# Kernel optimization log

Hardware: AMD Instinct MI355X
Metric: run time of the kernel (lower is better)

## Reference

```python
import jax, jax.numpy as jnp
import numpy as np

EMBED_DIM = 1024
FFN_DIM = 4096
N_QUBITS = 16
BATCH, SEQ = 4, 2048


def setup_inputs() -> dict:
    key = jax.random.key(0)
    ks = jax.random.split(key, 6)
    s1 = 1.0 / np.sqrt(EMBED_DIM)
    s2 = 1.0 / np.sqrt(FFN_DIM)
    s3 = 1.0 / np.sqrt(N_QUBITS)
    return {
        "x": jax.random.normal(ks[0], (BATCH, SEQ, EMBED_DIM), jnp.float32),
        "W1": jax.random.normal(ks[1], (FFN_DIM, EMBED_DIM), jnp.float32) * s1,
        "Wq": jax.random.normal(ks[2], (N_QUBITS, FFN_DIM), jnp.float32) * s2,
        "theta": jax.random.normal(ks[3], (N_QUBITS,), jnp.float32),
        "W2": jax.random.normal(ks[4], (FFN_DIM, N_QUBITS), jnp.float32) * s3,
        "Wo": jax.random.normal(ks[5], (EMBED_DIM, FFN_DIM), jnp.float32) * s2,
    }


def reference(x, W1, Wq, theta, W2, Wo):
    # linear1: [b,s,e] @ [f,e]^T -> [b,s,f]
    h = jnp.einsum('bse,fe->bsf', x, W1)
    # to_qubits: [b,s,f] -> [b,s,q]
    q = jnp.einsum('bsf,qf->bsq', h, Wq)
    # Quantum circuit: RX(q_i) encoding then trainable RX(theta_i) per wire,
    # wires are unentangled product states -> <Z_i> = cos(q_i + theta_i).
    qm = jnp.cos(q + theta)
    # linear2 + relu
    h2 = jax.nn.relu(jnp.einsum('bsq,fq->bsf', qm, W2))
    # out_proj (dropout is identity in eval / p=0)
    return jnp.einsum('bsf,ef->bse', h2, Wo)
```

## Files before the change

kernel.cpp:

```cpp
#include <hip/hip_runtime.h>
#include <hip/hip_bf16.h>
#include <math.h>

typedef _Float16 f16;
typedef __attribute__((ext_vector_type(8))) _Float16 f16x8;
typedef __attribute__((ext_vector_type(4))) _Float16 f16x4;
typedef __attribute__((ext_vector_type(4))) float f32x4;

#define M_TOT 8192
#define E_DIM 1024
#define F_DIM 4096
#define NQ    16

#define BARRIER() asm volatile("s_barrier" ::: "memory")
#define WAITV(n)  asm volatile("s_waitcnt vmcnt(" #n ")" ::: "memory")
#define WAITLGKM() asm volatile("s_waitcnt lgkmcnt(0)" ::: "memory")

__device__ __forceinline__ f16x8 cvt8(float4 a, float4 b) {
    f16x8 o;
    o[0] = (f16)a.x; o[1] = (f16)a.y; o[2] = (f16)a.z; o[3] = (f16)a.w;
    o[4] = (f16)b.x; o[5] = (f16)b.y; o[6] = (f16)b.z; o[7] = (f16)b.w;
    return o;
}

__global__ __launch_bounds__(256) void prep_kernel(
    const float* __restrict__ W1, f16* __restrict__ W1t,
    const float* __restrict__ wo, f16* __restrict__ woh,
    const float* __restrict__ W2, f16* __restrict__ w2p)
{
    __shared__ float ls[64][68];
    const int b = blockIdx.x;
    if (b < 1024) {
        const int bf = b & 63;
        const int be = b >> 6;
        const int t  = threadIdx.x;
        const int r  = t >> 4;
        const int c4 = (t & 15) * 4;
        #pragma unroll
        for (int i = 0; i < 4; ++i) {
            int fr = r + i * 16;
            float4 v = *reinterpret_cast<const float4*>(W1 + (size_t)(bf * 64 + fr) * E_DIM + be * 64 + c4);
            ls[fr][c4] = v.x; ls[fr][c4 + 1] = v.y; ls[fr][c4 + 2] = v.z; ls[fr][c4 + 3] = v.w;
        }
        __syncthreads();
        const int er = t >> 2;
        const int fc = (t & 3) * 16;
        f16x8 o0, o1;
        #pragma unroll
        for (int j = 0; j < 8; ++j) { o0[j] = (f16)ls[fc + j][er]; o1[j] = (f16)ls[fc + 8 + j][er]; }
        f16* dst = W1t + (size_t)(be * 64 + er) * F_DIM + bf * 64 + fc;
        *reinterpret_cast<f16x8*>(dst)     = o0;
        *reinterpret_cast<f16x8*>(dst + 8) = o1;
    } else if (b < 3072) {
        size_t i = ((size_t)(b - 1024) * 256 + threadIdx.x) * 8;
        float4 v0 = *reinterpret_cast<const float4*>(wo + i);
        float4 v1 = *reinterpret_cast<const float4*>(wo + i + 4);
        *reinterpret_cast<f16x8*>(woh + i) = cvt8(v0, v1);
    } else {
        int t = (b - 3072) * 256 + threadIdx.x;
        size_t i = (size_t)t * 8;
        int col = (int)(i & 31);
        f16x8 o;
        if (col < NQ) {
            int row = (int)(i >> 5);
            float4 v0 = *reinterpret_cast<const float4*>(W2 + (size_t)row * NQ + col);
            float4 v1 = *reinterpret_cast<const float4*>(W2 + (size_t)row * NQ + col + 4);
            o = cvt8(v0, v1);
        } else {
            for (int k = 0; k < 8; ++k) o[k] = (f16)0.f;
        }
        *reinterpret_cast<f16x8*>(w2p + i) = o;
    }
}

__global__ __launch_bounds__(256) void tg_kernel(
    const float* __restrict__ Wq, const f16* __restrict__ W1t,
    float* __restrict__ pT)
{
    const int w = threadIdx.x >> 6, lane = threadIdx.x & 63;
    const int fr = lane & 15, fq = lane >> 4;
    const int kc = blockIdx.x & 15;
    const int et = blockIdx.x >> 4;
    const int e0 = et * 128 + w * 32;
    const int kbase = kc * 256;

    f32x4 acc[2] = {};
    #pragma unroll
    for (int s = 0; s < 8; ++s) {
        int k = kbase + s * 32 + fq * 8;
        float4 a0 = *reinterpret_cast<const float4*>(Wq + (size_t)fr * F_DIM + k);
        float4 a1 = *reinterpret_cast<const float4*>(Wq + (size_t)fr * F_DIM + k + 4);
        f16x8 af = cvt8(a0, a1);
        #pragma unroll
        for (int n = 0; n < 2; ++n) {
            f16x8 bf = *reinterpret_cast<const f16x8*>(W1t + (size_t)(e0 + n * 16 + fr) * F_DIM + k);
            acc[n] = __builtin_amdgcn_mfma_f32_16x16x32_f16(af, bf, acc[n], 0, 0, 0);
        }
    }
    #pragma unroll
    for (int n = 0; n < 2; ++n)
        #pragma unroll
        for (int j = 0; j < 4; ++j)
            pT[(size_t)kc * (16 * E_DIM) + (size_t)(fq * 4 + j) * E_DIM + e0 + n * 16 + fr] = acc[n][j];
}

__global__ __launch_bounds__(256) void treduce_kernel(
    const float* __restrict__ pT, f16* __restrict__ Th)
{
    int idx = blockIdx.x * 256 + threadIdx.x;
    float s = 0.f;
    #pragma unroll
    for (int kc = 0; kc < 16; ++kc) s += pT[(size_t)kc * (16 * E_DIM) + idx];
    Th[idx] = (f16)s;
}

__global__ __launch_bounds__(512) void qx2_kernel(
    const float* __restrict__ x, const f16* __restrict__ Th,
    const float* __restrict__ theta, f16* __restrict__ qmp)
{
    __shared__ __align__(16) f16 ths[16 * 1024];
    __shared__ float pql[2048];
    const int tid = threadIdx.x, w = tid >> 6, lane = tid & 63;
    const int fr = lane & 15, fq = lane >> 4;
    const int m0 = blockIdx.x * 64;

    #pragma unroll
    for (int i = 0; i < 4; ++i) {
        int tau = i * 512 + tid;
        int q   = tau >> 7;
        int kb  = tau & 127;
        f16x8 v = *reinterpret_cast<const f16x8*>(Th + (size_t)q * E_DIM + kb * 8);
        int boff = (q * 2048 + kb * 16) ^ ((q & 7) << 4);
        *reinterpret_cast<f16x8*>((char*)ths + boff) = v;
    }
    __syncthreads();

    const int kc = w >> 2;
    const int rg = w & 3;
    const float* xa = x + (size_t)(m0 + rg * 16 + fr) * E_DIM + kc * 512;
    f32x4 acc = {};
    #pragma unroll
    for (int s = 0; s < 16; ++s) {
        int ko = s * 32 + fq * 8;
        float4 a0 = *reinterpret_cast<const float4*>(xa + ko);
        float4 a1 = *reinterpret_cast<const float4*>(xa + ko + 4);
        f16x8 af = cvt8(a0, a1);
        int boff = (fr * 2048 + (kc * 512 + ko) * 2) ^ ((fr & 7) << 4);
        f16x8 bf = *reinterpret_cast<const f16x8*>((char*)ths + boff);
        acc = __builtin_amdgcn_mfma_f32_16x16x32_f16(af, bf, acc, 0, 0, 0);
    }
    #pragma unroll
    for (int j = 0; j < 4; ++j)
        pql[(kc * 64 + rg * 16 + fq * 4 + j) * 16 + fr] = acc[j];
    __syncthreads();

    #pragma unroll
    for (int e = 0; e < 2; ++e) {
        int idx = e * 512 + tid;
        int row = idx >> 4, q = idx & 15;
        float s = pql[idx] + pql[1024 + idx];
        float v = cosf(s + theta[q]);
        qmp[(size_t)(m0 + row) * 32 + q]      = (f16)v;
        qmp[(size_t)(m0 + row) * 32 + 16 + q] = (f16)0.f;
    }
}

__device__ __forceinline__ void gload_lds16(const f16* g, f16* l) {
    __builtin_amdgcn_global_load_lds(
        (const __attribute__((address_space(1))) void*)(g),
        (__attribute__((address_space(3))) void*)(l), 16, 0, 0);
}

__global__ __launch_bounds__(512, 2)
void gemm4f(const f16* __restrict__ qmp, const f16* __restrict__ w2p,
            const f16* __restrict__ Wo, f16* __restrict__ P0, f16* __restrict__ P1)
{
    extern __shared__ __align__(16) f16 smem[];
    const int tid  = threadIdx.x;
    const int w    = tid >> 6;
    const int lane = tid & 63;

    const int bid = blockIdx.x;
    const int bx    = bid & 3;
    const int split = (bid >> 2) & 1;
    const int by    = bid >> 3;
    const int m0 = by * 256, n0 = bx * 256;

    const int wr = w >> 2, wc = w & 3;
    const int fr = lane & 15, fq = lane >> 4;
    const int K = 2048;

    const f16* Bb  = Wo + (size_t)split * K;
    const f16* w2g = w2p + (size_t)split * K * 32;
    f16* Pout = split ? P1 : P0;

    const int r0w = w * 32 + fr;
    f16x8 qreg0 = *reinterpret_cast<const f16x8*>(qmp + (size_t)(m0 + r0w) * 32 + fq * 8);
    f16x8 qreg1 = *reinterpret_cast<const f16x8*>(qmp + (size_t)(m0 + r0w + 16) * 32 + fq * 8);

    const int rl   = w * 8 + (lane >> 3);
    const int scol = (((lane & 7) ^ (rl & 7)) * 8);
    const f16* gB = Bb + (size_t)(n0 + rl) * F_DIM + scol;
    f16* lB = smem + 16384 + w * 512;

#define SB(b,h,j,kt) gload_lds16(gB + (size_t)((h)*128 + (j)*64) * F_DIM + (kt), lB + (b)*32768 + (h)*8192 + (j)*4096)
#define SBH(b,h,kt) do { SB(b,h,0,kt); SB(b,h,1,kt); } while(0)

    f16x8 w2a[4], w2b[4];
#define LOADW2(R, kt) do { _Pragma("unroll") \
    for (int ft = 0; ft < 4; ++ft) \
        R[ft] = *reinterpret_cast<const f16x8*>(w2g + (size_t)((kt) + ft*16 + fr) * 32 + fq * 8); } while(0)

#define PRODUCE(bdst, W2R) do {                                                   \
    f32x4 z_ = {0.f, 0.f, 0.f, 0.f};                                              \
    _Pragma("unroll") for (int ft = 0; ft < 4; ++ft) {                            \
        f32x4 c0_ = __builtin_amdgcn_mfma_f32_16x16x32_f16(W2R[ft], qreg0, z_, 0, 0, 0); \
        f32x4 c1_ = __builtin_amdgcn_mfma_f32_16x16x32_f16(W2R[ft], qreg1, z_, 0, 0, 0); \
        f16x4 h0_, h1_;                                                           \
        _Pragma("unroll") for (int jj = 0; jj < 4; ++jj) {                        \
            h0_[jj] = (f16)fmaxf(c0_[jj], 0.f); h1_[jj] = (f16)fmaxf(c1_[jj], 0.f); } \
        const int sl_ = (2 * ft + (fq >> 1)) ^ (fr & 7);                          \
        *reinterpret_cast<f16x4*>(smem + (bdst)*32768 + (r0w)*64      + sl_*8 + ((fq & 1) << 2)) = h0_; \
        *reinterpret_cast<f16x4*>(smem + (bdst)*32768 + (r0w+16)*64   + sl_*8 + ((fq & 1) << 2)) = h1_; \
    } } while(0)

    const int xm  = fr & 7;
    const int so0 = ((0 + fq) ^ xm) * 8;
    const int so1 = ((4 + fq) ^ xm) * 8;
    const int aro = (wr * 128 + fr) * 64;
    const int bro = (wc * 64  + fr) * 64;

#define AF(b,m,ks) (*reinterpret_cast<const f16x8*>(smem + (b)*32768 + aro + (m)*1024 + so##ks))
#define BF(b,n,ks) (*reinterpret_cast<const f16x8*>(smem + (b)*32768 + 16384 + bro + (n)*1024 + so##ks))

    f32x4 acc[8][4] = {};
    f16x8 bf[4][2];

#define PHASE(b, p, STAGES, W4) do {                                              \
    f16x8 a00 = AF(b, 2*(p),   0), a01 = AF(b, 2*(p),   1);                       \
    f16x8 a10 = AF(b, 2*(p)+1, 0), a11 = AF(b, 2*(p)+1, 1);                       \
    if ((p) == 0) { _Pragma("unroll")                                             \
        for (int n = 0; n < 4; ++n) { bf[n][0] = BF(b,n,0); bf[n][1] = BF(b,n,1); } } \
    STAGES;                                                                       \
    BARRIER();                                                                    \
    __builtin_amdgcn_s_setprio(1);                                                \
    _Pragma("unroll") for (int n = 0; n < 4; ++n) {                               \
        acc[2*(p)  ][n] = __builtin_amdgcn_mfma_f32_16x16x32_f16(a00, bf[n][0], acc[2*(p)  ][n], 0,0,0); \
        acc[2*(p)+1][n] = __builtin_amdgcn_mfma_f32_16x16x32_f16(a10, bf[n][0], acc[2*(p)+1][n], 0,0,0); } \
    _Pragma("unroll") for (int n = 0; n < 4; ++n) {                               \
        acc[2*(p)  ][n] = __builtin_amdgcn_mfma_f32_16x16x32_f16(a01, bf[n][1], acc[2*(p)  ][n], 0,0,0); \
        acc[2*(p)+1][n] = __builtin_amdgcn_mfma_f32_16x16x32_f16(a11, bf[n][1], acc[2*(p)+1][n], 0,0,0); } \
    __builtin_amdgcn_s_setprio(0);                                                \
    if (W4) { WAITV(8); WAITLGKM(); }                                             \
    BARRIER(); } while(0)

    const int NT = K >> 6;
    const int NI = NT >> 1;

    LOADW2(w2b, 0);
    LOADW2(w2a, 64);
    SBH(0,0,0);  SBH(0,1,0);
    SBH(1,0,64); SBH(1,1,64);
    WAITV(0);
    BARRIER();
    PRODUCE(0, w2b);
    WAITLGKM();
    BARRIER();

    for (int i = 0; i < NI; ++i) {
        int t2 = 2*i+2; if (t2 > NT-1) t2 = NT-1;
        int t3 = 2*i+3; if (t3 > NT-1) t3 = NT-1;
        const int k2 = t2 << 6, k3 = t3 << 6;
        PHASE(0, 0, PRODUCE(1, w2a),            0);
        PHASE(0, 1, LOADW2(w2b, k2); SBH(0,0,k2), 0);
        PHASE(0, 2, SBH(0,1,k2),                0);
        PHASE(0, 3, ,                           1);
        PHASE(1, 0, PRODUCE(0, w2b),            0);
        PHASE(1, 1, LOADW2(w2a, k3); SBH(1,0,k3), 0);
        PHASE(1, 2, SBH(1,1,k3),                0);
        PHASE(1, 3, ,                           1);
    }
    WAITV(0);

    #pragma unroll
    for (int m = 0; m < 8; ++m) {
        #pragma unroll
        for (int n = 0; n < 4; ++n) {
            #pragma unroll
            for (int j = 0; j < 4; ++j) {
                int row = m0 + wr * 128 + m * 16 + fq * 4 + j;
                int col = n0 + wc * 64  + n * 16 + fr;
                Pout[(size_t)row * E_DIM + col] = (f16)acc[m][n][j];
            }
        }
    }
#undef SB
#undef SBH
#undef LOADW2
#undef PRODUCE
#undef AF
#undef BF
#undef PHASE
}

__global__ __launch_bounds__(256) void out_reduce2_kernel(
    float* __restrict__ out, const f16* __restrict__ p0, const f16* __restrict__ p1)
{
    size_t i = ((size_t)blockIdx.x * 256 + threadIdx.x) * 8;
    f16x8 a = *reinterpret_cast<const f16x8*>(p0 + i);
    f16x8 b = *reinterpret_cast<const f16x8*>(p1 + i);
    float4 v0, v1;
    v0.x = (float)a[0] + (float)b[0]; v0.y = (float)a[1] + (float)b[1];
    v0.z = (float)a[2] + (float)b[2]; v0.w = (float)a[3] + (float)b[3];
    v1.x = (float)a[4] + (float)b[4]; v1.y = (float)a[5] + (float)b[5];
    v1.z = (float)a[6] + (float)b[6]; v1.w = (float)a[7] + (float)b[7];
    *reinterpret_cast<float4*>(out + i)     = v0;
    *reinterpret_cast<float4*>(out + i + 4) = v1;
}

extern "C" void kernel_launch(void* const* d_in, const int* in_sizes, int n_in,
                              void* d_out, int out_size, void* d_ws, size_t ws_size,
                              hipStream_t stream) {
    const float* x  = (const float*)d_in[0];
    const float* W1 = (const float*)d_in[1];
    const float* Wq = (const float*)d_in[2];
    const float* th = (const float*)d_in[3];
    const float* W2 = (const float*)d_in[4];
    const float* Wo = (const float*)d_in[5];
    float* out = (float*)d_out;

    char* base = (char*)d_ws;
    float* pT  = (float*)base;
    f16*   Th  = (f16*)(base + (1 << 20));
    f16*   w1t = (f16*)(base + 16777216);
    f16*   woh = w1t + (size_t)E_DIM * F_DIM;
    f16*   w2p = woh + (size_t)E_DIM * F_DIM;
    f16*   qmp = w2p + (size_t)F_DIM * 32;
    f16*   p0  = qmp + (size_t)M_TOT * 32;
    f16*   p1  = p0  + (size_t)M_TOT * E_DIM;

    static bool attr_done = false;
    if (!attr_done) {
        hipFuncSetAttribute((const void*)&gemm4f,
                            hipFuncAttributeMaxDynamicSharedMemorySize, 131072);
        attr_done = true;
    }

    prep_kernel<<<3136, 256, 0, stream>>>(W1, w1t, Wo, woh, W2, w2p);
    tg_kernel<<<128, 256, 0, stream>>>(Wq, w1t, pT);
    treduce_kernel<<<64, 256, 0, stream>>>(pT, Th);
    qx2_kernel<<<128, 512, 0, stream>>>(x, Th, th, qmp);
    gemm4f<<<256, 512, 131072, stream>>>(qmp, w2p, woh, p0, p1);
    out_reduce2_kernel<<<4096, 256, 0, stream>>>(out, p0, p1);
}
```

Baseline: 114.6 us.

## Fuse split-K reduction into GEMM epilogue via ticket/ready flags

Drops the separate out_reduce2 kernel. The two split-K blocks for each output tile now take a ticket with an atomic. The first block writes fp32 partials to a workspace and sets a ready flag, and the second spins on that flag, then adds the partials to its accumulators and writes the output. This saves a kernel launch and the fp16 partial round trip. In exchange it adds a spin-wait that depends on both blocks being co-resident, plus fp32 partial traffic. Partials are now fp32 instead of fp16.

```diff
diff --git a/kernel.cpp b/kernel.cpp
--- a/kernel.cpp
+++ b/kernel.cpp
@@ -26,7 +26,8 @@
 __global__ __launch_bounds__(256) void prep_kernel(
     const float* __restrict__ W1, f16* __restrict__ W1t,
     const float* __restrict__ wo, f16* __restrict__ woh,
-    const float* __restrict__ W2, f16* __restrict__ w2p)
+    const float* __restrict__ W2, f16* __restrict__ w2p,
+    int* __restrict__ flags)
 {
     __shared__ float ls[64][68];
     const int b = blockIdx.x;
@@ -56,7 +57,7 @@
         float4 v0 = *reinterpret_cast<const float4*>(wo + i);
         float4 v1 = *reinterpret_cast<const float4*>(wo + i + 4);
         *reinterpret_cast<f16x8*>(woh + i) = cvt8(v0, v1);
-    } else {
+    } else if (b < 3136) {
         int t = (b - 3072) * 256 + threadIdx.x;
         size_t i = (size_t)t * 8;
         int col = (int)(i & 31);
@@ -70,6 +71,8 @@
             for (int k = 0; k < 8; ++k) o[k] = (f16)0.f;
         }
         *reinterpret_cast<f16x8*>(w2p + i) = o;
+    } else {
+        if (threadIdx.x < 256) flags[threadIdx.x] = 0;
     }
 }
 
@@ -173,7 +176,8 @@
 
 __global__ __launch_bounds__(512, 2)
 void gemm4f(const f16* __restrict__ qmp, const f16* __restrict__ w2p,
-            const f16* __restrict__ Wo, f16* __restrict__ P0, f16* __restrict__ P1)
+            const f16* __restrict__ Wo, float* __restrict__ out,
+            float* __restrict__ pS, int* __restrict__ ticketF, int* __restrict__ readyF)
 {
     extern __shared__ __align__(16) f16 smem[];
     const int tid  = threadIdx.x;
@@ -192,7 +196,6 @@
 
     const f16* Bb  = Wo + (size_t)split * K;
     const f16* w2g = w2p + (size_t)split * K * 32;
-    f16* Pout = split ? P1 : P0;
 
     const int r0w = w * 32 + fr;
     f16x8 qreg0 = *reinterpret_cast<const f16x8*>(qmp + (size_t)(m0 + r0w) * 32 + fq * 8);
@@ -282,17 +285,46 @@
     }
     WAITV(0);
 
-    #pragma unroll
-    for (int m = 0; m < 8; ++m) {
-        #pragma unroll
-        for (int n = 0; n < 4; ++n) {
+    const int tile = (by << 2) | bx;
+    __shared__ int role_s;
+    if (tid == 0) role_s = atomicAdd(&ticketF[tile], 1);
+    __syncthreads();
+    const int role = role_s;
+    float* pT_ = pS + ((size_t)m0 * E_DIM + n0);
+
+    if (role == 0) {
+        #pragma unroll
+        for (int m = 0; m < 8; ++m)
             #pragma unroll
-            for (int j = 0; j < 4; ++j) {
-                int row = m0 + wr * 128 + m * 16 + fq * 4 + j;
-                int col = n0 + wc * 64  + n * 16 + fr;
-                Pout[(size_t)row * E_DIM + col] = (f16)acc[m][n][j];
-            }
+            for (int n = 0; n < 4; ++n)
+                #pragma unroll
+                for (int j = 0; j < 4; ++j) {
+                    int rl_ = wr * 128 + m * 16 + fq * 4 + j;
+                    int cl_ = wc * 64  + n * 16 + fr;
+                    pT_[(size_t)rl_ * E_DIM + cl_] = acc[m][n][j];
+                }
+        __threadfence();
+        __syncthreads();
+        if (tid == 0)
+            __hip_atomic_store(&readyF[tile], 1, __ATOMIC_RELEASE, __HIP_MEMORY_SCOPE_AGENT);
+    } else {
+        if (tid == 0) {
+            while (__hip_atomic_load(&readyF[tile], __ATOMIC_ACQUIRE, __HIP_MEMORY_SCOPE_AGENT) == 0)
+                __builtin_amdgcn_s_sleep(8);
         }
+        __syncthreads();
+        __threadfence();
+        #pragma unroll
+        for (int m = 0; m < 8; ++m)
+            #pragma unroll
+            for (int n = 0; n < 4; ++n)
+                #pragma unroll
+                for (int j = 0; j < 4; ++j) {
+                    int rl_ = wr * 128 + m * 16 + fq * 4 + j;
+                    int cl_ = wc * 64  + n * 16 + fr;
+                    out[(size_t)(m0 + rl_) * E_DIM + n0 + cl_] =
+                        acc[m][n][j] + pT_[(size_t)rl_ * E_DIM + cl_];
+                }
     }
 #undef SB
 #undef SBH
@@ -301,21 +333,6 @@
 #undef AF
 #undef BF
 #undef PHASE
-}
-
-__global__ __launch_bounds__(256) void out_reduce2_kernel(
-    float* __restrict__ out, const f16* __restrict__ p0, const f16* __restrict__ p1)
-{
-    size_t i = ((size_t)blockIdx.x * 256 + threadIdx.x) * 8;
-    f16x8 a = *reinterpret_cast<const f16x8*>(p0 + i);
-    f16x8 b = *reinterpret_cast<const f16x8*>(p1 + i);
-    float4 v0, v1;
-    v0.x = (float)a[0] + (float)b[0]; v0.y = (float)a[1] + (float)b[1];
-    v0.z = (float)a[2] + (float)b[2]; v0.w = (float)a[3] + (float)b[3];
-    v1.x = (float)a[4] + (float)b[4]; v1.y = (float)a[5] + (float)b[5];
-    v1.z = (float)a[6] + (float)b[6]; v1.w = (float)a[7] + (float)b[7];
-    *reinterpret_cast<float4*>(out + i)     = v0;
-    *reinterpret_cast<float4*>(out + i + 4) = v1;
 }
 
 extern "C" void kernel_launch(void* const* d_in, const int* in_sizes, int n_in,
@@ -332,12 +349,14 @@
     char* base = (char*)d_ws;
     float* pT  = (float*)base;
     f16*   Th  = (f16*)(base + (1 << 20));
+    int*   flags = (int*)(base + (1 << 20) + (1 << 16));
     f16*   w1t = (f16*)(base + 16777216);
     f16*   woh = w1t + (size_t)E_DIM * F_DIM;
     f16*   w2p = woh + (size_t)E_DIM * F_DIM;
     f16*   qmp = w2p + (size_t)F_DIM * 32;
-    f16*   p0  = qmp + (size_t)M_TOT * 32;
-    f16*   p1  = p0  + (size_t)M_TOT * E_DIM;
+    float* pS  = (float*)(qmp + (size_t)M_TOT * 32);
+    int*   ticketF = flags;
+    int*   readyF  = flags + 128;
 
     static bool attr_done = false;
     if (!attr_done) {
@@ -346,10 +365,9 @@
         attr_done = true;
     }
 
-    prep_kernel<<<3136, 256, 0, stream>>>(W1, w1t, Wo, woh, W2, w2p);
+    prep_kernel<<<3137, 256, 0, stream>>>(W1, w1t, Wo, woh, W2, w2p, flags);
     tg_kernel<<<128, 256, 0, stream>>>(Wq, w1t, pT);
     treduce_kernel<<<64, 256, 0, stream>>>(pT, Th);
     qx2_kernel<<<128, 512, 0, stream>>>(x, Th, th, qmp);
-    gemm4f<<<256, 512, 131072, stream>>>(qmp, w2p, woh, p0, p1);
-    out_reduce2_kernel<<<4096, 256, 0, stream>>>(out, p0, p1);
-}
+    gemm4f<<<256, 512, 131072, stream>>>(qmp, w2p, woh, out, pS, ticketF, readyF);
+}
```

Measured after the change: 259.9 us. 2.27x slower.
